# Performance work log

Hardware: AMD Instinct MI355X
Metric: run time of the kernel (lower is better)

## Reference

```python
import jax, jax.numpy as jnp
import numpy as np

H, D = 20, 64  # heads, head_dim (hidden_size = 1280)


def setup_inputs() -> dict:
    key = jax.random.key(0)
    ks = jax.random.split(key, 10)
    B, S, HID, CROSS, T_TXT, T_IP = 8, 4096, 1280, 2048, 77, 4
    w = lambda k, shp: jax.random.normal(k, shp, dtype=jnp.float32) * 0.02
    return {
        "hidden_states": jax.random.normal(ks[0], (B, S, HID), dtype=jnp.float32),
        "encoder_hidden_states": jax.random.normal(ks[1], (B, T_TXT, CROSS), dtype=jnp.float32),
        "ip_hidden_states": jax.random.normal(ks[2], (B, T_IP, CROSS), dtype=jnp.float32),
        "Wq": w(ks[3], (HID, HID)),
        "Wk": w(ks[4], (CROSS, HID)),
        "Wv": w(ks[5], (CROSS, HID)),
        "Wk_ip": w(ks[6], (CROSS, HID)),
        "Wv_ip": w(ks[7], (CROSS, HID)),
        "Wo": w(ks[8], (HID, HID)),
        "bo": jnp.zeros((HID,), dtype=jnp.float32),
    }


def _attend(q, kv_in, Wk, Wv):
    # q: [B,S,H,D]; kv_in: [B,T,cross]
    B, T = kv_in.shape[0], kv_in.shape[1]
    k = (kv_in @ Wk).reshape(B, T, H, D)
    v = (kv_in @ Wv).reshape(B, T, H, D)
    scale = 1.0 / jnp.sqrt(jnp.asarray(D, q.dtype))
    scores = jnp.einsum("bqhd,bkhd->bhqk", q, k) * scale
    probs = jax.nn.softmax(scores, axis=-1)
    out = jnp.einsum("bhqk,bkhd->bqhd", probs, v)
    return out.reshape(B, q.shape[1], H * D)


def reference(hidden_states, encoder_hidden_states, ip_hidden_states,
              Wq, Wk, Wv, Wk_ip, Wv_ip, Wo, bo):
    B, S, _ = hidden_states.shape
    q = (hidden_states @ Wq).reshape(B, S, H, D)
    # text cross-attention branch
    out = _attend(q, encoder_hidden_states, Wk, Wv)
    # IP-adapter branch (single adapter, scale=1.0, no mask)
    ip_scale = 1.0
    out = out + ip_scale * _attend(q, ip_hidden_states, Wk_ip, Wv_ip)
    # output projection (dropout is identity at inference)
    return out @ Wo + bo
```

## Files before the change

### kernel.cpp

```cpp
#include <hip/hip_runtime.h>

using u16 = unsigned short;
using u32 = unsigned int;
typedef __bf16 bf16x8 __attribute__((ext_vector_type(8)));
typedef float f32x4 __attribute__((ext_vector_type(4)));
typedef float f32x16 __attribute__((ext_vector_type(16)));

__device__ __forceinline__ u16 f2bf(float f) {
  u32 u = __float_as_uint(f);
  u += 0x7FFFu + ((u >> 16) & 1u);
  return (u16)(u >> 16);
}

__device__ __forceinline__ u32 cvtpk(float a, float b) {
  u32 r;
  asm("v_cvt_pk_bf16_f32 %0, %1, %2" : "=v"(r) : "v"(a), "v"(b));
  return r;
}

__device__ __forceinline__ void gload16(const u16* g, u16* l) {
  __builtin_amdgcn_global_load_lds((const __attribute__((address_space(1))) void*)g,
                                   (__attribute__((address_space(3))) void*)l, 16, 0, 0);
}

__global__ void f32_to_bf16_vec(const float* __restrict__ in, u16* __restrict__ out, long n4) {
  const long i = (long)blockIdx.x * 256 + threadIdx.x;
  if (i >= n4) return;
  const float4 v = ((const float4*)in)[i];
  ushort4 o;
  o.x = f2bf(v.x); o.y = f2bf(v.y); o.z = f2bf(v.z); o.w = f2bf(v.w);
  ((ushort4*)out)[i] = o;
}

__global__ void build_a_all(const float* __restrict__ enc, const float* __restrict__ ip,
                            u16* __restrict__ out) {
  const int i = blockIdx.x * 256 + threadIdx.x;
  const int row = i >> 9;
  const int c4 = i & 511;
  ushort4 o = {0, 0, 0, 0};
  const float4* src = nullptr;
  if (row < 616) src = (const float4*)enc + (size_t)row * 512 + c4;
  else if (row >= 640 && row < 672) src = (const float4*)ip + (size_t)(row - 640) * 512 + c4;
  if (src) {
    const float4 v = *src;
    o.x = f2bf(v.x); o.y = f2bf(v.y); o.z = f2bf(v.z); o.w = f2bf(v.w);
  }
  ((ushort4*)out)[i] = o;
}

__global__ void transpose_w4(const float* __restrict__ s0, const float* __restrict__ s1,
                             const float* __restrict__ s2, const float* __restrict__ s3,
                             u16* __restrict__ dst) {
  __shared__ float tile[32][33];
  const int z = blockIdx.z;
  const float* in = (z == 0) ? s0 : (z == 1) ? s1 : (z == 2) ? s2 : s3;
  u16* out = dst + (size_t)z * 1280 * 2048;
  const int K = 2048, N = 1280;
  const int n0 = blockIdx.x << 5, k0 = blockIdx.y << 5;
  const int x = threadIdx.x, y = threadIdx.y;
#pragma unroll
  for (int i = 0; i < 32; i += 8)
    tile[y + i][x] = in[(size_t)(k0 + y + i) * N + n0 + x];
  __syncthreads();
#pragma unroll
  for (int i = 0; i < 32; i += 8)
    out[(size_t)(n0 + y + i) * K + k0 + x] = f2bf(tile[x][y + i]);
}

__global__ void transpose_w2(const float* __restrict__ s0, const float* __restrict__ s1,
                             u16* __restrict__ d0, u16* __restrict__ d1) {
  __shared__ float tile[32][33];
  const int z = blockIdx.z;
  const float* in = z ? s1 : s0;
  u16* out = z ? d1 : d0;
  const int K = 1280, N = 1280;
  const int n0 = blockIdx.x << 5, k0 = blockIdx.y << 5;
  const int x = threadIdx.x, y = threadIdx.y;
#pragma unroll
  for (int i = 0; i < 32; i += 8)
    tile[y + i][x] = in[(size_t)(k0 + y + i) * N + n0 + x];
  __syncthreads();
#pragma unroll
  for (int i = 0; i < 32; i += 8)
    out[(size_t)(n0 + y + i) * K + k0 + x] = f2bf(tile[x][y + i]);
}

#define MFMA16(a, b, c) __builtin_amdgcn_mfma_f32_16x16x32_bf16(a, b, c, 0, 0, 0)
#define MFMA32(a, b, c) __builtin_amdgcn_mfma_f32_32x32x16_bf16(a, b, c, 0, 0, 0)

template <int MODE>
__global__ __launch_bounds__(512, 2) void gemm256(
    const u16* __restrict__ A, const u16* __restrict__ Bt,
    u16* __restrict__ Cb, float* __restrict__ Cf, const float* __restrict__ bias,
    const u16* __restrict__ kvcP, const u16* __restrict__ vtP,
    int M, int N, int K) {
  __shared__ __align__(16) u16 smem[67584];
  u16* As = smem;
  u16* Bs = smem + 32768;

  const int tid = threadIdx.x;
  const int w = tid >> 6, lane = tid & 63;
  const int lo = lane & 15, hi = lane >> 4;
  const int wm = w >> 2, wn = w & 3;

  const int nbn = N >> 8;
  int wg = blockIdx.x;
  {
    const int nwg = gridDim.x;
    const int q = nwg >> 3, r = nwg & 7;
    const int xcd = wg & 7, l = wg >> 3;
    wg = (xcd < r ? xcd * (q + 1) : r * (q + 1) + (xcd - r) * q) + l;
  }
  const int bm = wg / nbn, bn = wg % nbn;
  const int m0 = bm << 8, n0 = bn << 8;
  const int NT = K >> 6;

  const int sr = lane >> 3;
  const int sc8 = ((lane & 7) ^ sr) << 3;
  const u16* pA[2];
  const u16* pB[2];
#pragma unroll
  for (int i = 0; i < 2; ++i) {
    const int rr = (i * 8 + w) * 8 + sr;
    pA[i] = A + (size_t)(m0 + rr) * K + sc8;
    pB[i] = Bt + (size_t)(n0 + rr) * K + sc8;
  }
  const int ch0 = w * 512, ch1 = (8 + w) * 512;

#define STAGE_A(h, tt)                                                     \
  {                                                                        \
    const int ttc = ((tt) < NT) ? (tt) : (NT - 1);                         \
    u16* d = As + ((((tt)&1) * 2 + (h)) << 13);                            \
    const size_t off = (size_t)(h)*128 * K + (size_t)ttc * 64;             \
    gload16(pA[0] + off, d + ch0);                                         \
    gload16(pA[1] + off, d + ch1);                                         \
  }
#define STAGE_B(h, tt)                                                     \
  {                                                                        \
    const int ttc = ((tt) < NT) ? (tt) : (NT - 1);                         \
    u16* d = Bs + ((((tt)&1) * 2 + (h)) << 13);                            \
    const size_t off = (size_t)(h)*128 * K + (size_t)ttc * 64;             \
    gload16(pB[0] + off, d + ch0);                                         \
    gload16(pB[1] + off, d + ch1);                                         \
  }

  const int low0 = (lo << 7) | ((hi ^ (lo & 7)) << 4);
  const int low1 = (lo << 7) | (((4 | hi) ^ (lo & 7)) << 4);

  f32x4 acc[8][4];
#pragma unroll
  for (int i = 0; i < 8; ++i)
#pragma unroll
    for (int j = 0; j < 4; ++j) acc[i][j] = (f32x4){0.f, 0.f, 0.f, 0.f};

  STAGE_B(0, 0); STAGE_B(1, 0);
  STAGE_A(0, 0); STAGE_A(1, 0);
  STAGE_B(0, 1); STAGE_B(1, 1);

  const char* aSm = (const char*)As;
  const char* bSm = (const char*)Bs;

  for (int t = 0; t < NT; ++t) {
    const int p = t & 1;
    const int aBase = (p * 2 + wm) << 14;
    const int bBase = ((p * 2 + (wn >> 1)) << 14) + ((wn & 1) << 13);

    asm volatile("s_waitcnt vmcnt(4)" ::: "memory");
    asm volatile("s_barrier" ::: "memory");

    bf16x8 a0[4][2], a1[4][2], b0[2][2], b1[2][2];
#pragma unroll
    for (int mf = 0; mf < 4; ++mf) {
      a0[mf][0] = *(const bf16x8*)(aSm + aBase + (mf << 11) + low0);
      a0[mf][1] = *(const bf16x8*)(aSm + aBase + (mf << 11) + low1);
    }
#pragma unroll
    for (int nf = 0; nf < 2; ++nf) {
      b0[nf][0] = *(const bf16x8*)(bSm + bBase + (nf << 11) + low0);
      b0[nf][1] = *(const bf16x8*)(bSm + bBase + (nf << 11) + low1);
    }
    STAGE_A(0, t + 1);
    __builtin_amdgcn_s_setprio(1);
#pragma unroll
    for (int mf = 0; mf < 4; ++mf)
#pragma unroll
      for (int nf = 0; nf < 2; ++nf) {
        acc[mf][nf] = MFMA16(a0[mf][0], b0[nf][0], acc[mf][nf]);
        acc[mf][nf] = MFMA16(a0[mf][1], b0[nf][1], acc[mf][nf]);
      }
    __builtin_amdgcn_s_setprio(0);

#pragma unroll
    for (int nf = 0; nf < 2; ++nf) {
      b1[nf][0] = *(const bf16x8*)(bSm + bBase + (1 << 12) + (nf << 11) + low0);
      b1[nf][1] = *(const bf16x8*)(bSm + bBase + (1 << 12) + (nf << 11) + low1);
    }
    STAGE_A(1, t + 1);
    __builtin_amdgcn_s_setprio(1);
#pragma unroll
    for (int mf = 0; mf < 4; ++mf)
#pragma unroll
      for (int nf = 0; nf < 2; ++nf) {
        acc[mf][2 + nf] = MFMA16(a0[mf][0], b1[nf][0], acc[mf][2 + nf]);
        acc[mf][2 + nf] = MFMA16(a0[mf][1], b1[nf][1], acc[mf][2 + nf]);
      }
    __builtin_amdgcn_s_setprio(0);
    asm volatile("s_barrier" ::: "memory");

#pragma unroll
    for (int mf = 0; mf < 4; ++mf) {
      a1[mf][0] = *(const bf16x8*)(aSm + aBase + (1 << 13) + (mf << 11) + low0);
      a1[mf][1] = *(const bf16x8*)(aSm + aBase + (1 << 13) + (mf << 11) + low1);
    }
    STAGE_B(0, t + 2);
    __builtin_amdgcn_s_setprio(1);
#pragma unroll
    for (int mf = 0; mf < 4; ++mf)
#pragma unroll
      for (int nf = 0; nf < 2; ++nf) {
        acc[4 + mf][nf] = MFMA16(a1[mf][0], b0[nf][0], acc[4 + mf][nf]);
        acc[4 + mf][nf] = MFMA16(a1[mf][1], b0[nf][1], acc[4 + mf][nf]);
      }
    __builtin_amdgcn_s_setprio(0);

    STAGE_B(1, t + 2);
    __builtin_amdgcn_s_setprio(1);
#pragma unroll
    for (int mf = 0; mf < 4; ++mf)
#pragma unroll
      for (int nf = 0; nf < 2; ++nf) {
        acc[4 + mf][2 + nf] = MFMA16(a1[mf][0], b1[nf][0], acc[4 + mf][2 + nf]);
        acc[4 + mf][2 + nf] = MFMA16(a1[mf][1], b1[nf][1], acc[4 + mf][2 + nf]);
      }
    __builtin_amdgcn_s_setprio(0);
  }

  if (MODE != 2) {
#pragma unroll
    for (int g = 0; g < 2; ++g)
#pragma unroll
      for (int mf = 0; mf < 4; ++mf)
#pragma unroll
        for (int ng = 0; ng < 2; ++ng)
#pragma unroll
          for (int nfi = 0; nfi < 2; ++nfi) {
            const f32x4 v = acc[g * 4 + mf][ng * 2 + nfi];
            const int row0 = m0 + wm * 128 + g * 64 + mf * 16 + hi * 4;
            const int col = n0 + wn * 64 + ng * 32 + nfi * 16 + lo;
            if (MODE == 1) {
              const float bb = bias[col];
#pragma unroll
              for (int r = 0; r < 4; ++r)
                Cf[(size_t)(row0 + r) * N + col] = v[r] + bb;
            } else {
#pragma unroll
              for (int r = 0; r < 4; ++r)
                Cb[(size_t)(row0 + r) * N + col] = f2bf(v[r]);
            }
          }
  } else {
    const int l31 = lane & 31, hi5 = lane >> 5;
    const int h = bn * 4 + wn;
    const int b = m0 >> 12;

    bf16x8 kreg[3][4];
#pragma unroll
    for (int kf = 0; kf < 3; ++kf) {
      const int key = kf * 32 + l31;
      const u16* kp;
      if (key < 77) kp = kvcP + (size_t)(b * 77 + key) * 5120 + h * 64 + hi5 * 8;
      else if (key >= 80 && key < 84)
        kp = kvcP + (size_t)(640 + b * 4 + key - 80) * 5120 + 2560 + h * 64 + hi5 * 8;
      else kp = kvcP + h * 64 + hi5 * 8;
#pragma unroll
      for (int dc = 0; dc < 4; ++dc) kreg[kf][dc] = *(const bf16x8*)(kp + dc * 16);
    }

    asm volatile("s_waitcnt vmcnt(0)" ::: "memory");
    __builtin_amdgcn_s_barrier();

    u16* qlds = smem + w * 8448;
#pragma unroll
    for (int g = 0; g < 2; ++g)
#pragma unroll
      for (int mf = 0; mf < 4; ++mf)
#pragma unroll
        for (int ng = 0; ng < 2; ++ng)
#pragma unroll
          for (int nfi = 0; nfi < 2; ++nfi) {
            const f32x4 v = acc[g * 4 + mf][ng * 2 + nfi];
            const int qrow = g * 64 + mf * 16 + hi * 4;
            const int d = ng * 32 + nfi * 16 + lo;
#pragma unroll
            for (int r = 0; r < 4; ++r) qlds[(qrow + r) * 66 + d] = f2bf(v[r]);
          }

    const u16* vbase = vtP + ((size_t)(b * 20 + h) * 64) * 96 + hi5 * 8;
    const int rowB = m0 + wm * 128;

#pragma unroll
    for (int pass = 0; pass < 2; ++pass) {
      bf16x8 qf0[4], qf1[4];
#pragma unroll
      for (int dc = 0; dc < 4; ++dc) {
        qf0[dc] = *(const bf16x8*)&qlds[(pass * 64 + l31) * 66 + dc * 16 + hi5 * 8];
        qf1[dc] = *(const bf16x8*)&qlds[(pass * 64 + 32 + l31) * 66 + dc * 16 + hi5 * 8];
      }

      f32x16 s0[3], s1[3];
#pragma unroll
      for (int kf = 0; kf < 3; ++kf)
#pragma unroll
        for (int r = 0; r < 16; ++r) { s0[kf][r] = 0.f; s1[kf][r] = 0.f; }

#pragma unroll
      for (int kf = 0; kf < 3; ++kf)
#pragma unroll
        for (int dc = 0; dc < 4; ++dc) {
          s0[kf] = MFMA32(kreg[kf][dc], qf0[dc], s0[kf]);
          s1[kf] = MFMA32(kreg[kf][dc], qf1[dc], s1[kf]);
        }

      float st0 = 0.f, si0 = 0.f, st1 = 0.f, si1 = 0.f;
#pragma unroll
      for (int kf = 0; kf < 3; ++kf)
#pragma unroll
        for (int r = 0; r < 16; ++r) {
          const int krem = (r & 3) + 8 * (r >> 2);
          const int k = kf * 32 + krem + 4 * hi5;
          const bool vtx = k < 77;
          const bool vip = (k >= 80) & (k < 84);
          const float e0 = (vtx | vip) ? __expf(s0[kf][r] * 0.125f) : 0.f;
          const float e1 = (vtx | vip) ? __expf(s1[kf][r] * 0.125f) : 0.f;
          s0[kf][r] = e0; s1[kf][r] = e1;
          st0 += vtx ? e0 : 0.f; si0 += vip ? e0 : 0.f;
          st1 += vtx ? e1 : 0.f; si1 += vip ? e1 : 0.f;
        }
      st0 += __shfl_xor(st0, 32); si0 += __shfl_xor(si0, 32);
      st1 += __shfl_xor(st1, 32); si1 += __shfl_xor(si1, 32);
      const float rt0 = __fdividef(1.f, st0), ri0 = __fdividef(1.f, si0);
      const float rt1 = __fdividef(1.f, st1), ri1 = __fdividef(1.f, si1);
#pragma unroll
      for (int kf = 0; kf < 3; ++kf)
#pragma unroll
        for (int r = 0; r < 16; ++r) {
          const int krem = (r & 3) + 8 * (r >> 2);
          const int k = kf * 32 + krem + 4 * hi5;
          const bool vip = (k >= 80) & (k < 84);
          s0[kf][r] *= vip ? ri0 : rt0;
          s1[kf][r] *= vip ? ri1 : rt1;
        }

#define PV_STORE(sA, qoff)                                                  \
      {                                                                     \
        f32x16 pacc[2];                                                     \
        _Pragma("unroll") for (int nf = 0; nf < 2; ++nf)                    \
        _Pragma("unroll") for (int r = 0; r < 16; ++r) pacc[nf][r] = 0.f;   \
        _Pragma("unroll") for (int ks = 0; ks < 6; ++ks) {                  \
          const int kf = ks >> 1;                                           \
          const int rb = (ks & 1) * 8;                                      \
          const u32 lo01 = cvtpk(sA[kf][rb + 0], sA[kf][rb + 1]);           \
          const u32 lo23 = cvtpk(sA[kf][rb + 2], sA[kf][rb + 3]);           \
          const u32 hi01 = cvtpk(sA[kf][rb + 4], sA[kf][rb + 5]);           \
          const u32 hi23 = cvtpk(sA[kf][rb + 6], sA[kf][rb + 7]);           \
          const u32 plo01 = __shfl_xor(lo01, 32);                           \
          const u32 plo23 = __shfl_xor(lo23, 32);                           \
          const u32 phi01 = __shfl_xor(hi01, 32);                           \
          const u32 phi23 = __shfl_xor(hi23, 32);                           \
          union { u32 u[4]; bf16x8 v; } pu;                                 \
          pu.u[0] = hi5 ? phi01 : lo01;                                     \
          pu.u[1] = hi5 ? phi23 : lo23;                                     \
          pu.u[2] = hi5 ? hi01 : plo01;                                     \
          pu.u[3] = hi5 ? hi23 : plo23;                                     \
          _Pragma("unroll") for (int nf = 0; nf < 2; ++nf) {                \
            const bf16x8 vb = *(const bf16x8*)(vbase +                      \
                (size_t)(nf * 32 + l31) * 96 + ks * 16);                    \
            pacc[nf] = MFMA32(pu.v, vb, pacc[nf]);                          \
          }                                                                 \
        }                                                                   \
        _Pragma("unroll") for (int nf = 0; nf < 2; ++nf)                    \
        _Pragma("unroll") for (int r = 0; r < 16; ++r) {                    \
          const int row = rowB + pass * 64 + (qoff) +                       \
                          (r & 3) + 8 * (r >> 2) + 4 * hi5;                 \
          Cb[(size_t)row * 1280 + h * 64 + nf * 32 + l31] =                 \
              f2bf(pacc[nf][r]);                                            \
        }                                                                   \
      }

      PV_STORE(s0, 0)
      PV_STORE(s1, 32)
#undef PV_STORE
    }
  }
#undef STAGE_A
#undef STAGE_B
}

__global__ __launch_bounds__(256) void build_vt(const u16* __restrict__ kvc,
                                                u16* __restrict__ vt) {
  __shared__ u16 Ls[96][72];
  const int tid = threadIdx.x;
  const int h = blockIdx.x % 20, b = blockIdx.x / 20;
  for (int idx = tid; idx < 96 * 8; idx += 256) {
    const int row = idx >> 3, c8 = (idx & 7) << 3;
    uint4 val = make_uint4(0, 0, 0, 0);
    if (row < 77)
      val = *(const uint4*)(kvc + (size_t)(b * 77 + row) * 5120 + 1280 + h * 64 + c8);
    else if (row >= 80 && row < 84)
      val = *(const uint4*)(kvc + (size_t)(640 + b * 4 + row - 80) * 5120 + 3840 + h * 64 + c8);
    *(uint4*)&Ls[row][c8] = val;
  }
  __syncthreads();
  u16* dst = vt + (size_t)blockIdx.x * 64 * 96;
  for (int idx = tid; idx < 768; idx += 256) {
    const int d = idx / 12, c = (idx % 12) * 8;
    u16 tmp[8];
#pragma unroll
    for (int j = 0; j < 8; ++j) tmp[j] = Ls[c + j][d];
    *(uint4*)(dst + d * 96 + c) = *(const uint4*)tmp;
  }
}

extern "C" void kernel_launch(void* const* d_in, const int* in_sizes, int n_in,
                              void* d_out, int out_size, void* d_ws, size_t ws_size,
                              hipStream_t stream) {
  (void)in_sizes; (void)n_in; (void)out_size; (void)ws_size;
  const float* hs   = (const float*)d_in[0];
  const float* enc  = (const float*)d_in[1];
  const float* ip   = (const float*)d_in[2];
  const float* Wq   = (const float*)d_in[3];
  const float* Wk   = (const float*)d_in[4];
  const float* Wv   = (const float*)d_in[5];
  const float* Wkip = (const float*)d_in[6];
  const float* Wvip = (const float*)d_in[7];
  const float* Wo   = (const float*)d_in[8];
  const float* bo   = (const float*)d_in[9];
  float* out = (float*)d_out;

  u16* wq_t  = (u16*)d_out;
  u16* hs_bf = (u16*)d_out + 41943040;

  char* ws = (char*)d_ws;
  u16* kvc   = (u16*)(ws);
  u16* wo_t  = (u16*)(ws + 15728640);
  u16* vt    = (u16*)(ws + 19005440);
  u16* attn  = (u16*)(ws + 20971520);
  u16* kvw   = (u16*)(ws + 20971520 + 3276800);
  u16* a_all = (u16*)(ws + 20971520 + 24248320);

  f32_to_bf16_vec<<<40960, 256, 0, stream>>>(hs, hs_bf, 10485760);
  build_a_all<<<1536, 256, 0, stream>>>(enc, ip, a_all);

  dim3 tb(32, 8);
  transpose_w4<<<dim3(40, 64, 4), tb, 0, stream>>>(Wk, Wv, Wkip, Wvip, kvw);
  transpose_w2<<<dim3(40, 40, 2), tb, 0, stream>>>(Wq, Wo, wq_t, wo_t);

  gemm256<0><<<60, 512, 0, stream>>>(a_all, kvw, kvc, nullptr, nullptr, nullptr, nullptr,
                                     768, 5120, 2048);
  build_vt<<<160, 256, 0, stream>>>(kvc, vt);

  gemm256<2><<<640, 512, 0, stream>>>(hs_bf, wq_t, attn, nullptr, nullptr, kvc, vt,
                                      32768, 1280, 1280);

  gemm256<1><<<640, 512, 0, stream>>>(attn, wo_t, nullptr, out, bo, nullptr, nullptr,
                                      32768, 1280, 1280);
}
```

Before: 373.7 us.

## Fuse fp32-to-bf16 conversion of hidden states into Q-projection GEMM A loads

Removes the standalone hidden-state fp32-to-bf16 conversion kernel. The Q GEMM now loads fp32 A tiles into registers two stages ahead, converts them with packed bf16 conversion and writes them to LDS, instead of using async global-to-LDS copies of a precomputed bf16 buffer. This avoids writing and re-reading the 80 MB bf16 intermediate, at the cost of extra registers, VALU conversion work and synchronous LDS writes inside the GEMM pipeline. The fp32 A reads also double the A-side global traffic within the GEMM.

```diff
diff --git a/kernel.cpp b/kernel.cpp
--- a/kernel.cpp
+++ b/kernel.cpp
@@ -21,15 +21,6 @@
 __device__ __forceinline__ void gload16(const u16* g, u16* l) {
   __builtin_amdgcn_global_load_lds((const __attribute__((address_space(1))) void*)g,
                                    (__attribute__((address_space(3))) void*)l, 16, 0, 0);
-}
-
-__global__ void f32_to_bf16_vec(const float* __restrict__ in, u16* __restrict__ out, long n4) {
-  const long i = (long)blockIdx.x * 256 + threadIdx.x;
-  if (i >= n4) return;
-  const float4 v = ((const float4*)in)[i];
-  ushort4 o;
-  o.x = f2bf(v.x); o.y = f2bf(v.y); o.z = f2bf(v.z); o.w = f2bf(v.w);
-  ((ushort4*)out)[i] = o;
 }
 
 __global__ void build_a_all(const float* __restrict__ enc, const float* __restrict__ ip,
@@ -88,9 +79,9 @@
 #define MFMA16(a, b, c) __builtin_amdgcn_mfma_f32_16x16x32_bf16(a, b, c, 0, 0, 0)
 #define MFMA32(a, b, c) __builtin_amdgcn_mfma_f32_32x32x16_bf16(a, b, c, 0, 0, 0)
 
-template <int MODE>
+template <int MODE, int AF32>
 __global__ __launch_bounds__(512, 2) void gemm256(
-    const u16* __restrict__ A, const u16* __restrict__ Bt,
+    const u16* __restrict__ A, const float* __restrict__ Af, const u16* __restrict__ Bt,
     u16* __restrict__ Cb, float* __restrict__ Cf, const float* __restrict__ bias,
     const u16* __restrict__ kvcP, const u16* __restrict__ vtP,
     int M, int N, int K) {
@@ -117,6 +108,7 @@
 
   const int sr = lane >> 3;
   const int sc8 = ((lane & 7) ^ sr) << 3;
+  const int c8l = (lane & 7) << 3;
   const u16* pA[2];
   const u16* pB[2];
 #pragma unroll
@@ -144,6 +136,34 @@
     gload16(pB[1] + off, d + ch1);                                         \
   }
 
+  float4 fAr[2][2][2];
+#define LOADA_F32(tt)                                                      \
+  {                                                                        \
+    const int ttc = ((tt) < NT) ? (tt) : (NT - 1);                         \
+    _Pragma("unroll") for (int h = 0; h < 2; ++h)                          \
+    _Pragma("unroll") for (int i = 0; i < 2; ++i) {                        \
+      const int rr = (i * 8 + w) * 8 + sr;                                 \
+      const float* s = Af + (size_t)(m0 + h * 128 + rr) * K +              \
+                       (size_t)ttc * 64 + c8l;                             \
+      fAr[h][i][0] = *(const float4*)s;                                    \
+      fAr[h][i][1] = *(const float4*)(s + 4);                              \
+    }                                                                      \
+  }
+#define WRITEA(tt)                                                         \
+  {                                                                        \
+    _Pragma("unroll") for (int h = 0; h < 2; ++h)                          \
+    _Pragma("unroll") for (int i = 0; i < 2; ++i) {                        \
+      const int rr = (i * 8 + w) * 8 + sr;                                 \
+      u16* d = As + ((((tt)&1) * 2 + h) << 13) + rr * 64 + sc8;            \
+      union { u32 u[4]; bf16x8 v; } pk;                                    \
+      pk.u[0] = cvtpk(fAr[h][i][0].x, fAr[h][i][0].y);                     \
+      pk.u[1] = cvtpk(fAr[h][i][0].z, fAr[h][i][0].w);                     \
+      pk.u[2] = cvtpk(fAr[h][i][1].x, fAr[h][i][1].y);                     \
+      pk.u[3] = cvtpk(fAr[h][i][1].z, fAr[h][i][1].w);                     \
+      *(bf16x8*)d = pk.v;                                                  \
+    }                                                                      \
+  }
+
   const int low0 = (lo << 7) | ((hi ^ (lo & 7)) << 4);
   const int low1 = (lo << 7) | (((4 | hi) ^ (lo & 7)) << 4);
 
@@ -153,9 +173,18 @@
 #pragma unroll
     for (int j = 0; j < 4; ++j) acc[i][j] = (f32x4){0.f, 0.f, 0.f, 0.f};
 
-  STAGE_B(0, 0); STAGE_B(1, 0);
-  STAGE_A(0, 0); STAGE_A(1, 0);
-  STAGE_B(0, 1); STAGE_B(1, 1);
+  if (AF32) {
+    LOADA_F32(0);
+    STAGE_B(0, 0); STAGE_B(1, 0);
+    asm volatile("s_waitcnt vmcnt(4)" ::: "memory");
+    WRITEA(0);
+    LOADA_F32(1);
+    STAGE_B(0, 1); STAGE_B(1, 1);
+  } else {
+    STAGE_B(0, 0); STAGE_B(1, 0);
+    STAGE_A(0, 0); STAGE_A(1, 0);
+    STAGE_B(0, 1); STAGE_B(1, 1);
+  }
 
   const char* aSm = (const char*)As;
   const char* bSm = (const char*)Bs;
@@ -165,8 +194,13 @@
     const int aBase = (p * 2 + wm) << 14;
     const int bBase = ((p * 2 + (wn >> 1)) << 14) + ((wn & 1) << 13);
 
-    asm volatile("s_waitcnt vmcnt(4)" ::: "memory");
+    asm volatile("s_waitcnt vmcnt(4) lgkmcnt(0)" ::: "memory");
     asm volatile("s_barrier" ::: "memory");
+
+    if (AF32) {
+      WRITEA(t + 1);
+      LOADA_F32(t + 2);
+    }
 
     bf16x8 a0[4][2], a1[4][2], b0[2][2], b1[2][2];
 #pragma unroll
@@ -179,7 +213,7 @@
       b0[nf][0] = *(const bf16x8*)(bSm + bBase + (nf << 11) + low0);
       b0[nf][1] = *(const bf16x8*)(bSm + bBase + (nf << 11) + low1);
     }
-    STAGE_A(0, t + 1);
+    if (!AF32) STAGE_A(0, t + 1);
     __builtin_amdgcn_s_setprio(1);
 #pragma unroll
     for (int mf = 0; mf < 4; ++mf)
@@ -195,7 +229,7 @@
       b1[nf][0] = *(const bf16x8*)(bSm + bBase + (1 << 12) + (nf << 11) + low0);
       b1[nf][1] = *(const bf16x8*)(bSm + bBase + (1 << 12) + (nf << 11) + low1);
     }
-    STAGE_A(1, t + 1);
+    if (!AF32) STAGE_A(1, t + 1);
     __builtin_amdgcn_s_setprio(1);
 #pragma unroll
     for (int mf = 0; mf < 4; ++mf)
@@ -394,6 +428,8 @@
   }
 #undef STAGE_A
 #undef STAGE_B
+#undef LOADA_F32
+#undef WRITEA
 }
 
 __global__ __launch_bounds__(256) void build_vt(const u16* __restrict__ kvc,
@@ -437,8 +473,7 @@
   const float* bo   = (const float*)d_in[9];
   float* out = (float*)d_out;
 
-  u16* wq_t  = (u16*)d_out;
-  u16* hs_bf = (u16*)d_out + 41943040;
+  u16* wq_t = (u16*)d_out;
 
   char* ws = (char*)d_ws;
   u16* kvc   = (u16*)(ws);
@@ -448,20 +483,19 @@
   u16* kvw   = (u16*)(ws + 20971520 + 3276800);
   u16* a_all = (u16*)(ws + 20971520 + 24248320);
 
-  f32_to_bf16_vec<<<40960, 256, 0, stream>>>(hs, hs_bf, 10485760);
   build_a_all<<<1536, 256, 0, stream>>>(enc, ip, a_all);
 
   dim3 tb(32, 8);
   transpose_w4<<<dim3(40, 64, 4), tb, 0, stream>>>(Wk, Wv, Wkip, Wvip, kvw);
   transpose_w2<<<dim3(40, 40, 2), tb, 0, stream>>>(Wq, Wo, wq_t, wo_t);
 
-  gemm256<0><<<60, 512, 0, stream>>>(a_all, kvw, kvc, nullptr, nullptr, nullptr, nullptr,
-                                     768, 5120, 2048);
+  gemm256<0, 0><<<60, 512, 0, stream>>>(a_all, nullptr, kvw, kvc, nullptr, nullptr,
+                                        nullptr, nullptr, 768, 5120, 2048);
   build_vt<<<160, 256, 0, stream>>>(kvc, vt);
 
-  gemm256<2><<<640, 512, 0, stream>>>(hs_bf, wq_t, attn, nullptr, nullptr, kvc, vt,
-                                      32768, 1280, 1280);
-
-  gemm256<1><<<640, 512, 0, stream>>>(attn, wo_t, nullptr, out, bo, nullptr, nullptr,
-                                      32768, 1280, 1280);
-}
+  gemm256<2, 1><<<640, 512, 0, stream>>>(nullptr, hs, wq_t, attn, nullptr, nullptr,
+                                         kvc, vt, 32768, 1280, 1280);
+
+  gemm256<1, 0><<<640, 512, 0, stream>>>(attn, nullptr, wo_t, nullptr, out, bo,
+                                         nullptr, nullptr, 32768, 1280, 1280);
+}
```

After: 385.0 us. 1.03x slower.
